# Performance work log

Hardware: AMD Instinct MI355X
Metric: run time of the kernel (lower is better)

The kernel has to match this reference:

```python
import jax, jax.numpy as jnp
import numpy as np

B, TP, TQ, DP, DQ, H, AH = 32, 512, 64, 256, 256, 256, 256
NL = 2  # len(nhids)
NEG = -1e9


def setup_inputs() -> dict:
    key = jax.random.key(0)
    ks = jax.random.split(key, 12)
    s = 0.05  # small init scale (stands in for xavier uniform)
    inp = {
        'input_p': jax.random.normal(ks[0], (B, TP, DP), jnp.float32),
        'mask_p': jnp.ones((B, TP), jnp.float32),
        'input_q': jax.random.normal(ks[1], (B, TQ, DQ), jnp.float32),
        'mask_q': jnp.ones((B, TQ), jnp.float32),
        # Match-LSTM attention params, stacked over depth (layer0 input dim DP == nhids[0] == 256)
        'W_att_p': jax.random.normal(ks[2], (NL, DP, AH), jnp.float32) * s,
        'W_att_q': jax.random.normal(ks[3], (NL, DQ, AH), jnp.float32) * s,
        'W_att_r': jax.random.normal(ks[4], (NL, H, AH), jnp.float32) * s,
        'w_att':   jax.random.normal(ks[5], (NL, AH), jnp.float32) * s,
        # LSTMCell: pre_act_linear over cat([input(=in_dim+DQ), h]) -> 4H; in_dim+DQ+H = 768 for both layers
        'W_lstm':  jax.random.normal(ks[6], (NL, DP + DQ + H, 4 * H), jnp.float32) * s,
        'bias_f':  jnp.ones((NL, H), jnp.float32),        # init.fill_(1.0)
        'bias_iog': jnp.zeros((NL, 3 * H), jnp.float32),  # init.fill_(0.0)
    }
    return inp


def reference(input_p, mask_p, input_q, mask_q,
              W_att_p, W_att_q, W_att_r, w_att,
              W_lstm, bias_f, bias_iog):
    bsz = input_p.shape[0]
    qmask_big = mask_q > 0  # (B,TQ) bool, reused every step
    x = input_p  # layer input, (B, TP, Din)
    for d in range(NL):
        qWq = jnp.einsum('btq,qa->bta', input_q, W_att_q[d])  # precompute (B,TQ,AH)
        Wp, Wr, wa = W_att_p[d], W_att_r[d], w_att[d]
        Wl = W_lstm[d]
        bias = jnp.concatenate([bias_f[d], bias_iog[d]])  # order: f | i,o,g

        def step(carry, xt_mt):
            h, c = carry
            xt, mt = xt_mt  # (B,Din), (B,)
            # match attention over query
            s = jnp.tanh(qWq + (xt @ Wp + h @ Wr)[:, None, :]) @ wa  # (B,TQ)
            alpha = jax.nn.softmax(jnp.where(qmask_big, s, NEG), axis=-1)
            z = jnp.einsum('bt,btd->bd', alpha, input_q)  # (B,DQ)
            # LSTM cell: pre_act over cat([attn_input, h])
            pre = jnp.concatenate([xt, z, h], axis=-1) @ Wl + bias
            f, i, o, g = jnp.split(pre, 4, axis=-1)
            m = mt[:, None]
            c1 = jax.nn.sigmoid(f) * c + jax.nn.sigmoid(i) * jnp.tanh(g)
            c1 = c1 * m + c * (1.0 - m)
            h1 = jax.nn.sigmoid(o) * jnp.tanh(c1)
            h1 = h1 * m + h * (1.0 - m)
            return (h1, c1), h1

        h0 = jnp.zeros((bsz, H), input_p.dtype)
        c0 = jnp.zeros((bsz, H), input_p.dtype)
        xs = (jnp.swapaxes(x, 0, 1), jnp.swapaxes(mask_p, 0, 1))  # time-major
        _, hs = jax.lax.scan(step, (h0, c0), xs)  # hs: (TP, B, H)
        x = jnp.swapaxes(hs, 0, 1)  # (B, TP, H), fed to next layer (dropout p=0)
    return x
```

## Files before the change

### kernel.cpp

```cpp
#include <hip/hip_runtime.h>
#include <hip/hip_bf16.h>


#define NB 32
#define TPL 512
#define TQL 64
#define DD 256
#define H4 1024
#define NC 1280
#define NS 8
#define SC 160
#define GC 128

typedef unsigned long long u64;

__device__ __forceinline__ float fast_tanh(float x) {
  float xc = fminf(fmaxf(x, -9.f), 9.f);
  float e = __expf(2.f * xc);
  return (e - 1.f) * __builtin_amdgcn_rcpf(e + 1.f);
}
__device__ __forceinline__ float fast_sigmoid(float x) {
  return __builtin_amdgcn_rcpf(1.f + __expf(-x));
}
__device__ __forceinline__ float bflo(unsigned int w) { return __uint_as_float(w << 16); }
__device__ __forceinline__ float bfhi(unsigned int w) { return __uint_as_float(w & 0xffff0000u); }
__device__ __forceinline__ unsigned int packbf(float a, float b) {
  unsigned int lo = __hip_bfloat16_raw(__float2bfloat16(a)).x;
  unsigned int hi = __hip_bfloat16_raw(__float2bfloat16(b)).x;
  return lo | (hi << 16);
}

__device__ __forceinline__ u64 aload64(const u64* p) {
  return __hip_atomic_load(p, __ATOMIC_RELAXED, __HIP_MEMORY_SCOPE_AGENT);
}
__device__ __forceinline__ void astore64(u64* p, u64 v) {
  __hip_atomic_store(p, v, __ATOMIC_RELAXED, __HIP_MEMORY_SCOPE_AGENT);
}
__device__ __forceinline__ u64 packsv(float val, unsigned int seq) {
  return ((u64)seq << 32) | (u64)__float_as_uint(val);
}
__device__ __forceinline__ float spinload(const u64* p, unsigned int seq) {
  u64 v = aload64(p);
  int guard = 0;
  while ((unsigned int)(v >> 32) != seq) {
    __builtin_amdgcn_s_sleep(1);
    v = aload64(p);
    if (++guard > (1 << 24)) break;
  }
  return __uint_as_float((unsigned int)v);
}

__device__ __forceinline__ int perm_col(int c) {
  if (c < DD) return (c >> 5) * SC + (c & 31);
  int cc = c - DD;
  int g = cc >> 8;
  int m = cc & 255;
  return (m >> 5) * SC + 32 + (g << 5) + (m & 31);
}

__global__ __launch_bounds__(256) void pack_weights(
    const float* __restrict__ Wp, const float* __restrict__ Wq,
    const float* __restrict__ Wl,
    float* __restrict__ wx, float* __restrict__ wqv)
{
  int d = blockIdx.y;
  int idx = blockIdx.x * 256 + threadIdx.x;
  if (idx >= DD * NC) return;
  int k = idx / NC, j = idx % NC;
  int o = d * DD * NC + idx;
  const float* Wld = Wl + (size_t)d * 768 * H4;
  if (j < DD) {
    int s = d * DD * DD + k * DD + j;
    wx[o] = Wp[s]; wqv[o] = Wq[s];
  } else {
    int c = j - DD;
    wx[o]  = Wld[(size_t)k * H4 + c];
    wqv[o] = Wld[(size_t)(DD + k) * H4 + c];
  }
}

__global__ __launch_bounds__(256) void pack_attl(
    const float* __restrict__ Wr, uint2* __restrict__ attl)
{
  int idx = blockIdx.x * 256 + threadIdx.x;
  if (idx >= 2 * NS * 4 * 512) return;
  int slot = idx & 511; int r = idx >> 9;
  int i = r & 3; r >>= 2;
  int j = r & 7; int d = r >> 3;
  int acol = slot & 31, ak = slot >> 5;
  int kq = ak * 4 + i;
  int col = (j << 5) + acol;
  float v[4];
  #pragma unroll
  for (int kr = 0; kr < 4; ++kr)
    v[kr] = Wr[((size_t)d * DD + kq * 4 + kr) * DD + col];
  attl[idx] = make_uint2(packbf(v[0], v[1]), packbf(v[2], v[3]));
}

__global__ __launch_bounds__(256) void pack_gatel(
    const float* __restrict__ Wl, uint2* __restrict__ gatel)
{
  int idx = blockIdx.x * 256 + threadIdx.x;
  if (idx >= 2 * NS * 16 * 512) return;
  int slot = idx & 511; int r = idx >> 9;
  int i = r & 15; r >>= 4;
  int j = r & 7; int d = r >> 3;
  int gcol = slot >> 2, gq = slot & 3;
  int kq = i * 4 + gq;
  int g = gcol >> 5, pos = gcol & 31;
  float v[4];
  #pragma unroll
  for (int kr = 0; kr < 4; ++kr) {
    int k = kq * 4 + kr;
    v[kr] = Wl[((size_t)d * 768 + 512 + k) * H4 + (g << 8) + (j << 5) + pos];
  }
  gatel[idx] = make_uint2(packbf(v[0], v[1]), packbf(v[2], v[3]));
}

template <bool PERM>
__global__ __launch_bounds__(256) void sgemm(
    const float* __restrict__ A, const float* __restrict__ Bm,
    float* __restrict__ C)
{
  __shared__ float As[16][65];
  __shared__ float Bs[16][64];
  int tid = threadIdx.x;
  int tx = tid & 15, ty = tid >> 4;
  int col0 = blockIdx.x * 64, row0 = blockIdx.y * 64;
  float acc[4][4] = {};
  for (int kt = 0; kt < DD; kt += 16) {
    #pragma unroll
    for (int i = 0; i < 4; ++i) {
      int e = tid + i * 256;
      As[e & 15][e >> 4] = A[(size_t)(row0 + (e >> 4)) * DD + kt + (e & 15)];
      Bs[e >> 6][e & 63] = Bm[(size_t)(kt + (e >> 6)) * NC + col0 + (e & 63)];
    }
    __syncthreads();
    #pragma unroll
    for (int kk = 0; kk < 16; ++kk) {
      float a[4], bv[4];
      #pragma unroll
      for (int i = 0; i < 4; ++i) a[i] = As[kk][ty * 4 + i];
      #pragma unroll
      for (int jj = 0; jj < 4; ++jj) bv[jj] = Bs[kk][tx * 4 + jj];
      #pragma unroll
      for (int i = 0; i < 4; ++i)
        #pragma unroll
        for (int jj = 0; jj < 4; ++jj)
          acc[i][jj] = fmaf(a[i], bv[jj], acc[i][jj]);
    }
    __syncthreads();
  }
  #pragma unroll
  for (int i = 0; i < 4; ++i)
    #pragma unroll
    for (int jj = 0; jj < 4; ++jj) {
      int c = col0 + tx * 4 + jj;
      int cc = PERM ? perm_col(c) : c;
      C[(size_t)(row0 + ty * 4 + i) * NC + cc] = acc[i][jj];
    }
}

__global__ __launch_bounds__(512, 1) void scan(
    const float* __restrict__ xpl,
    const float* __restrict__ qv,
    const uint2* __restrict__ attl,
    const uint2* __restrict__ gatel,
    const float* __restrict__ wa,
    const float* __restrict__ bias_f,
    const float* __restrict__ bias_iog,
    const float* __restrict__ mask_p,
    const float* __restrict__ mask_q,
    u64* __restrict__ xch_s,
    u64* __restrict__ xch_h,
    float* __restrict__ out,
    int lbase)
{
  const int bid = blockIdx.x;
  const int j = bid & 7, b = bid >> 3;
  const int tid = threadIdx.x;
  const int lane = tid & 63;

  __shared__ uint2 wg_l[16][512];
  __shared__ uint2 wat_l[4][512];
  __shared__ unsigned int vl_l[8][512];
  __shared__ float qT[32][65];
  __shared__ __align__(16) float h_lds[DD];
  __shared__ float xsl[SC];
  __shared__ float hw_att[32], waa[32], c_sh[32];
  __shared__ float att_part[16][33];
  __shared__ float sc_part[8][TQL];
  __shared__ float al_s[TQL];
  __shared__ float pre_s[GC], bias_s[GC];

  const float* qv_b = qv + (size_t)b * TQL * NC;
  u64* xch_s_b = xch_s + b * (NS * TQL);
  u64* xch_h_b = xch_h + b * DD;

  {
    const uint2* gp = gatel + (size_t)j * 16 * 512;
    for (int i = tid; i < 16 * 512; i += 512) wg_l[i >> 9][i & 511] = gp[i];
    const uint2* ap = attl + (size_t)j * 4 * 512;
    for (int i = tid; i < 4 * 512; i += 512) wat_l[i >> 9][i & 511] = ap[i];
    for (int i = tid; i < TQL * 32; i += 512) {
      int tq = i >> 5, a = i & 31;
      qT[a][tq] = qv_b[(size_t)tq * NC + (j << 5) + a];
    }
    for (int f = tid; f < 8 * 512; f += 512) {
      int ii = f >> 9, slot = f & 511;
      int gcol = slot >> 2, gq = slot & 3;
      int tw = gq * 8 + ii;
      int g = gcol >> 5, m = (j << 5) + (gcol & 31);
      float v0 = qv_b[(size_t)(2 * tw) * NC + DD + (g << 8) + m];
      float v1 = qv_b[(size_t)(2 * tw + 1) * NC + DD + (g << 8) + m];
      vl_l[ii][slot] = packbf(v0, v1);
    }
    if (tid < 32) { waa[tid] = wa[(j << 5) + tid]; c_sh[tid] = 0.f; }
    if (tid < GC) {
      int g = tid >> 5, m = (j << 5) + (tid & 31);
      bias_s[tid] = (g == 0) ? bias_f[m] : bias_iog[((g - 1) << 8) + m];
    }
  }
  float mq = mask_q[b * TQL + lane];
  __syncthreads();

  const int ak = tid >> 5;
  const int stq = tid & 63, ssub = tid >> 6;
  const int gcol = tid >> 2, gq = tid & 3;

  for (int t = 0; t < TPL; ++t) {
    const float* xrow = xpl + ((size_t)b * TPL + t) * NC + j * SC;
    float xv = (tid < SC) ? xrow[tid] : 0.f;
    const unsigned int hseq = (unsigned int)(lbase + t);
    const unsigned int sseq = (unsigned int)(lbase + t + 1);

    __syncthreads();
    if (tid < DD) h_lds[tid] = (t > 0) ? spinload(xch_h_b + tid, hseq) : 0.f;
    if (tid < SC) xsl[tid] = xv;
    __syncthreads();

    {
      float a0 = 0.f, a1 = 0.f;
      #pragma unroll
      for (int i = 0; i < 4; ++i) {
        int kq = ak * 4 + i;
        uint2 w = wat_l[i][tid];
        float4 h0 = *(const float4*)&h_lds[kq * 4];
        a0 = fmaf(h0.x, bflo(w.x), a0); a1 = fmaf(h0.y, bfhi(w.x), a1);
        a0 = fmaf(h0.z, bflo(w.y), a0); a1 = fmaf(h0.w, bfhi(w.y), a1);
      }
      att_part[ak][tid & 31] = a0 + a1;
    }
    __syncthreads();
    if (tid < 32) {
      float s = 0.f;
      #pragma unroll
      for (int i = 0; i < 16; ++i) s += att_part[i][tid];
      hw_att[tid] = s;
    }
    __syncthreads();

    {
      float p = 0.f;
      #pragma unroll
      for (int i = 0; i < 4; ++i) {
        int a = ssub * 4 + i;
        p = fmaf(fast_tanh(qT[a][stq] + xsl[a] + hw_att[a]), waa[a], p);
      }
      sc_part[ssub][stq] = p;
    }
    __syncthreads();
    if (tid < TQL) {
      float s = 0.f;
      #pragma unroll
      for (int q = 0; q < 8; ++q) s += sc_part[q][tid];
      astore64(xch_s_b + (j << 6) + tid, packsv(s, sseq));
    }

    float hwg;
    {
      float g0 = 0.f, g1 = 0.f;
      #pragma unroll
      for (int i = 0; i < 16; ++i) {
        int kq = i * 4 + gq;
        uint2 w = wg_l[i][tid];
        float4 h0 = *(const float4*)&h_lds[kq * 4];
        g0 = fmaf(h0.x, bflo(w.x), g0); g1 = fmaf(h0.y, bfhi(w.x), g1);
        g0 = fmaf(h0.z, bflo(w.y), g0); g1 = fmaf(h0.w, bfhi(w.y), g1);
      }
      hwg = g0 + g1;
      hwg += __shfl_xor(hwg, 1);
      hwg += __shfl_xor(hwg, 2);
    }

    __syncthreads();
    sc_part[ssub][stq] = spinload(xch_s_b + (ssub << 6) + stq, sseq);
    __syncthreads();
    if (tid < TQL) {
      float v = 0.f;
      #pragma unroll
      for (int q = 0; q < 8; ++q) v += sc_part[q][tid];
      v = (mq > 0.f) ? v : -1e9f;
      float m = v;
      #pragma unroll
      for (int off = 32; off > 0; off >>= 1) m = fmaxf(m, __shfl_xor(m, off));
      float p = __expf(v - m);
      float su = p;
      #pragma unroll
      for (int off = 32; off > 0; off >>= 1) su += __shfl_xor(su, off);
      al_s[tid] = p * __builtin_amdgcn_rcpf(su);
    }
    __syncthreads();

    {
      float d0 = 0.f, d1 = 0.f;
      #pragma unroll
      for (int i = 0; i < 8; ++i) {
        int tw = gq * 8 + i;
        unsigned int v = vl_l[i][tid];
        d0 = fmaf(al_s[2 * tw], bflo(v), d0);
        d1 = fmaf(al_s[2 * tw + 1], bfhi(v), d1);
      }
      float d = d0 + d1;
      d += __shfl_xor(d, 1);
      d += __shfl_xor(d, 2);
      if (gq == 0)
        pre_s[gcol] = hwg + d + xsl[32 + gcol] + bias_s[gcol];
    }
    __syncthreads();

    if (tid < 32) {
      float f  = pre_s[tid];
      float ii = pre_s[32 + tid];
      float oo = pre_s[64 + tid];
      float g  = pre_s[96 + tid];
      float mtv = mask_p[b * TPL + t];
      int m = (j << 5) + tid;
      float c0 = c_sh[tid], h0 = h_lds[m];
      float c1 = fast_sigmoid(f) * c0 + fast_sigmoid(ii) * fast_tanh(g);
      c1 = c1 * mtv + c0 * (1.f - mtv);
      float h1 = fast_sigmoid(oo) * fast_tanh(c1);
      h1 = h1 * mtv + h0 * (1.f - mtv);
      c_sh[tid] = c1;
      astore64(xch_h_b + m, packsv(h1, (unsigned int)(lbase + t + 1)));
      out[((size_t)b * TPL + t) * DD + m] = h1;
    }
  }
}

extern "C" void kernel_launch(void* const* d_in, const int* in_sizes, int n_in,
                              void* d_out, int out_size, void* d_ws, size_t ws_size,
                              hipStream_t stream) {
  const float* input_p  = (const float*)d_in[0];
  const float* mask_p   = (const float*)d_in[1];
  const float* input_q  = (const float*)d_in[2];
  const float* mask_q   = (const float*)d_in[3];
  const float* W_att_p  = (const float*)d_in[4];
  const float* W_att_q  = (const float*)d_in[5];
  const float* W_att_r  = (const float*)d_in[6];
  const float* w_att    = (const float*)d_in[7];
  const float* W_lstm   = (const float*)d_in[8];
  const float* bias_f   = (const float*)d_in[9];
  const float* bias_iog = (const float*)d_in[10];
  float* out = (float*)d_out;
  float* ws  = (float*)d_ws;
  (void)ws_size; (void)in_sizes; (void)n_in; (void)out_size;

  const size_t SZ_XPL  = (size_t)NB * TPL * NC;
  const size_t SZ_QV   = (size_t)NB * TQL * NC;
  const size_t SZ_W    = (size_t)DD * NC;
  const size_t SZ_ATTL = (size_t)NS * 4 * 512;
  const size_t SZ_GATL = (size_t)NS * 16 * 512;

  float* ws_xpl = ws;
  float* ws_qv  = ws_xpl + SZ_XPL;
  float* ws_wx  = ws_qv  + 2 * SZ_QV;
  float* ws_wqv = ws_wx  + 2 * SZ_W;
  float* ws_o0  = ws_wqv + 2 * SZ_W;
  uint2* ws_attl = (uint2*)(ws_o0 + (size_t)NB * TPL * DD);
  uint2* ws_gatl = ws_attl + 2 * SZ_ATTL;
  u64*   ws_xs   = (u64*)(ws_gatl + 2 * SZ_GATL);
  u64*   ws_xh   = ws_xs + NB * NS * TQL;

  dim3 gpack((DD * NC + 255) / 256, 2);
  pack_weights<<<gpack, 256, 0, stream>>>(W_att_p, W_att_q, W_lstm, ws_wx, ws_wqv);
  pack_attl<<<(2 * NS * 4 * 512 + 255) / 256, 256, 0, stream>>>(W_att_r, ws_attl);
  pack_gatel<<<(2 * NS * 16 * 512 + 255) / 256, 256, 0, stream>>>(W_lstm, ws_gatl);
  hipMemsetAsync(ws_xs, 0, (NB * NS * TQL + NB * DD) * sizeof(u64), stream);

  for (int d = 0; d < 2; ++d) {
    dim3 g(NC / 64, (NB * TQL) / 64);
    sgemm<false><<<g, 256, 0, stream>>>(input_q, ws_wqv + d * SZ_W, ws_qv + d * SZ_QV);
  }

  {
    dim3 g(NC / 64, (NB * TPL) / 64);
    sgemm<true><<<g, 256, 0, stream>>>(input_p, ws_wx, ws_xpl);
    scan<<<NB * NS, 512, 0, stream>>>(ws_xpl, ws_qv, ws_attl, ws_gatl,
                                      w_att, bias_f, bias_iog, mask_p, mask_q,
                                      ws_xs, ws_xh, ws_o0, 0);
  }
  {
    dim3 g(NC / 64, (NB * TPL) / 64);
    sgemm<true><<<g, 256, 0, stream>>>(ws_o0, ws_wx + SZ_W, ws_xpl);
    scan<<<NB * NS, 512, 0, stream>>>(ws_xpl, ws_qv + SZ_QV, ws_attl + SZ_ATTL,
                                      ws_gatl + SZ_GATL, w_att + DD, bias_f + DD,
                                      bias_iog + 3 * DD, mask_p, mask_q,
                                      ws_xs, ws_xh, out, TPL);
  }
}
```

Before: 4.021 ms.

## Process two batch rows per workgroup in the recurrent scan kernel

Each scan workgroup now handles two batch elements (b and b+16) for its column slice, halving the grid. LDS-resident weights are shared between the two rows, and the h/score exchange spinloads poll both rows together. Barriers are amortised over twice the work, and the cell state moves into a register. In exchange, the serial per-step compute in each workgroup roughly doubles, and LDS use grows.

```diff
diff --git a/kernel.cpp b/kernel.cpp
--- a/kernel.cpp
+++ b/kernel.cpp
@@ -39,15 +39,20 @@
 __device__ __forceinline__ u64 packsv(float val, unsigned int seq) {
   return ((u64)seq << 32) | (u64)__float_as_uint(val);
 }
-__device__ __forceinline__ float spinload(const u64* p, unsigned int seq) {
-  u64 v = aload64(p);
+__device__ __forceinline__ void spinload2(const u64* p0, const u64* p1,
+                                          unsigned int seq,
+                                          float* v0, float* v1) {
+  u64 a = aload64(p0);
+  u64 b = aload64(p1);
   int guard = 0;
-  while ((unsigned int)(v >> 32) != seq) {
+  while (((unsigned int)(a >> 32) != seq) || ((unsigned int)(b >> 32) != seq)) {
     __builtin_amdgcn_s_sleep(1);
-    v = aload64(p);
+    if ((unsigned int)(a >> 32) != seq) a = aload64(p0);
+    if ((unsigned int)(b >> 32) != seq) b = aload64(p1);
     if (++guard > (1 << 24)) break;
   }
-  return __uint_as_float((unsigned int)v);
+  *v0 = __uint_as_float((unsigned int)a);
+  *v1 = __uint_as_float((unsigned int)b);
 }
 
 __device__ __forceinline__ int perm_col(int c) {
@@ -176,52 +181,58 @@
     float* __restrict__ out,
     int lbase)
 {
-  const int bid = blockIdx.x;
-  const int j = bid & 7, b = bid >> 3;
+  const int wgid = blockIdx.x;
+  const int j = wgid & 7, pair = wgid >> 3;
   const int tid = threadIdx.x;
   const int lane = tid & 63;
+  const int bS0 = pair, bS1 = pair + 16;
 
   __shared__ uint2 wg_l[16][512];
   __shared__ uint2 wat_l[4][512];
-  __shared__ unsigned int vl_l[8][512];
-  __shared__ float qT[32][65];
-  __shared__ __align__(16) float h_lds[DD];
-  __shared__ float xsl[SC];
-  __shared__ float hw_att[32], waa[32], c_sh[32];
-  __shared__ float att_part[16][33];
-  __shared__ float sc_part[8][TQL];
-  __shared__ float al_s[TQL];
-  __shared__ float pre_s[GC], bias_s[GC];
-
-  const float* qv_b = qv + (size_t)b * TQL * NC;
-  u64* xch_s_b = xch_s + b * (NS * TQL);
-  u64* xch_h_b = xch_h + b * DD;
+  __shared__ unsigned int vl_l[2][8][512];
+  __shared__ float qT[2][32][65];
+  __shared__ __align__(16) float h_lds[2][DD];
+  __shared__ float xsl[2][SC];
+  __shared__ float hw_att[2][32], waa[32], c_dummy;
+  __shared__ float att_part[2][16][33];
+  __shared__ float sc_part[2][8][TQL];
+  __shared__ float al_s[2][TQL];
+  __shared__ float pre_s[2][GC], bias_s[GC];
+
+  const float* qvb[2] = { qv + (size_t)bS0 * TQL * NC,
+                          qv + (size_t)bS1 * TQL * NC };
+  u64* xsc[2] = { xch_s + bS0 * (NS * TQL), xch_s + bS1 * (NS * TQL) };
+  u64* xh[2]  = { xch_h + bS0 * DD,         xch_h + bS1 * DD };
 
   {
     const uint2* gp = gatel + (size_t)j * 16 * 512;
     for (int i = tid; i < 16 * 512; i += 512) wg_l[i >> 9][i & 511] = gp[i];
     const uint2* ap = attl + (size_t)j * 4 * 512;
     for (int i = tid; i < 4 * 512; i += 512) wat_l[i >> 9][i & 511] = ap[i];
-    for (int i = tid; i < TQL * 32; i += 512) {
-      int tq = i >> 5, a = i & 31;
-      qT[a][tq] = qv_b[(size_t)tq * NC + (j << 5) + a];
-    }
-    for (int f = tid; f < 8 * 512; f += 512) {
-      int ii = f >> 9, slot = f & 511;
-      int gcol = slot >> 2, gq = slot & 3;
-      int tw = gq * 8 + ii;
-      int g = gcol >> 5, m = (j << 5) + (gcol & 31);
-      float v0 = qv_b[(size_t)(2 * tw) * NC + DD + (g << 8) + m];
-      float v1 = qv_b[(size_t)(2 * tw + 1) * NC + DD + (g << 8) + m];
-      vl_l[ii][slot] = packbf(v0, v1);
-    }
-    if (tid < 32) { waa[tid] = wa[(j << 5) + tid]; c_sh[tid] = 0.f; }
+    #pragma unroll
+    for (int s = 0; s < 2; ++s) {
+      for (int i = tid; i < TQL * 32; i += 512) {
+        int tq = i >> 5, a = i & 31;
+        qT[s][a][tq] = qvb[s][(size_t)tq * NC + (j << 5) + a];
+      }
+      for (int f = tid; f < 8 * 512; f += 512) {
+        int ii = f >> 9, slot = f & 511;
+        int gcol = slot >> 2, gq = slot & 3;
+        int tw = gq * 8 + ii;
+        int g = gcol >> 5, m = (j << 5) + (gcol & 31);
+        float v0 = qvb[s][(size_t)(2 * tw) * NC + DD + (g << 8) + m];
+        float v1 = qvb[s][(size_t)(2 * tw + 1) * NC + DD + (g << 8) + m];
+        vl_l[s][ii][slot] = packbf(v0, v1);
+      }
+    }
+    if (tid < 32) waa[tid] = wa[(j << 5) + tid];
     if (tid < GC) {
       int g = tid >> 5, m = (j << 5) + (tid & 31);
       bias_s[tid] = (g == 0) ? bias_f[m] : bias_iog[((g - 1) << 8) + m];
     }
   }
-  float mq = mask_q[b * TQL + lane];
+  float mqv = (tid < 128) ? mask_q[((tid >> 6) ? bS1 : bS0) * TQL + lane] : 0.f;
+  float cv = 0.f;
   __syncthreads();
 
   const int ak = tid >> 5;
@@ -229,78 +240,102 @@
   const int gcol = tid >> 2, gq = tid & 3;
 
   for (int t = 0; t < TPL; ++t) {
-    const float* xrow = xpl + ((size_t)b * TPL + t) * NC + j * SC;
-    float xv = (tid < SC) ? xrow[tid] : 0.f;
+    const float* xrA = xpl + ((size_t)bS0 * TPL + t) * NC + j * SC;
+    const float* xrB = xpl + ((size_t)bS1 * TPL + t) * NC + j * SC;
+    float xv = 0.f;
+    if (tid < SC) xv = xrA[tid];
+    else if (tid < 2 * SC) xv = xrB[tid - SC];
+    float mtv = (tid < 64) ? mask_p[((lane >> 5) ? bS1 : bS0) * TPL + t] : 0.f;
     const unsigned int hseq = (unsigned int)(lbase + t);
     const unsigned int sseq = (unsigned int)(lbase + t + 1);
 
     __syncthreads();
-    if (tid < DD) h_lds[tid] = (t > 0) ? spinload(xch_h_b + tid, hseq) : 0.f;
-    if (tid < SC) xsl[tid] = xv;
-    __syncthreads();
-
-    {
+    if (tid < DD) {
+      float hA = 0.f, hB = 0.f;
+      if (t > 0) spinload2(xh[0] + tid, xh[1] + tid, hseq, &hA, &hB);
+      h_lds[0][tid] = hA;
+      h_lds[1][tid] = hB;
+    }
+    if (tid < SC) xsl[0][tid] = xv;
+    else if (tid < 2 * SC) xsl[1][tid - SC] = xv;
+    __syncthreads();
+
+    #pragma unroll
+    for (int s = 0; s < 2; ++s) {
       float a0 = 0.f, a1 = 0.f;
       #pragma unroll
       for (int i = 0; i < 4; ++i) {
         int kq = ak * 4 + i;
         uint2 w = wat_l[i][tid];
-        float4 h0 = *(const float4*)&h_lds[kq * 4];
+        float4 h0 = *(const float4*)&h_lds[s][kq * 4];
         a0 = fmaf(h0.x, bflo(w.x), a0); a1 = fmaf(h0.y, bfhi(w.x), a1);
         a0 = fmaf(h0.z, bflo(w.y), a0); a1 = fmaf(h0.w, bfhi(w.y), a1);
       }
-      att_part[ak][tid & 31] = a0 + a1;
-    }
-    __syncthreads();
-    if (tid < 32) {
-      float s = 0.f;
-      #pragma unroll
-      for (int i = 0; i < 16; ++i) s += att_part[i][tid];
-      hw_att[tid] = s;
-    }
-    __syncthreads();
-
-    {
+      att_part[s][ak][tid & 31] = a0 + a1;
+    }
+    __syncthreads();
+    if (tid < 64) {
+      int s = tid >> 5, e = tid & 31;
+      float sum = 0.f;
+      #pragma unroll
+      for (int i = 0; i < 16; ++i) sum += att_part[s][i][e];
+      hw_att[s][e] = sum;
+    }
+    __syncthreads();
+
+    #pragma unroll
+    for (int s = 0; s < 2; ++s) {
       float p = 0.f;
       #pragma unroll
       for (int i = 0; i < 4; ++i) {
         int a = ssub * 4 + i;
-        p = fmaf(fast_tanh(qT[a][stq] + xsl[a] + hw_att[a]), waa[a], p);
-      }
-      sc_part[ssub][stq] = p;
-    }
-    __syncthreads();
-    if (tid < TQL) {
-      float s = 0.f;
-      #pragma unroll
-      for (int q = 0; q < 8; ++q) s += sc_part[q][tid];
-      astore64(xch_s_b + (j << 6) + tid, packsv(s, sseq));
-    }
-
-    float hwg;
-    {
+        p = fmaf(fast_tanh(qT[s][a][stq] + xsl[s][a] + hw_att[s][a]),
+                 waa[a], p);
+      }
+      sc_part[s][ssub][stq] = p;
+    }
+    __syncthreads();
+    if (tid < 128) {
+      int s = tid >> 6;
+      float sum = 0.f;
+      #pragma unroll
+      for (int q = 0; q < 8; ++q) sum += sc_part[s][q][lane];
+      astore64(xsc[s] + (j << 6) + lane, packsv(sum, sseq));
+    }
+
+    float hwgA, hwgB;
+    #pragma unroll
+    for (int s = 0; s < 2; ++s) {
       float g0 = 0.f, g1 = 0.f;
       #pragma unroll
       for (int i = 0; i < 16; ++i) {
         int kq = i * 4 + gq;
         uint2 w = wg_l[i][tid];
-        float4 h0 = *(const float4*)&h_lds[kq * 4];
+        float4 h0 = *(const float4*)&h_lds[s][kq * 4];
         g0 = fmaf(h0.x, bflo(w.x), g0); g1 = fmaf(h0.y, bfhi(w.x), g1);
         g0 = fmaf(h0.z, bflo(w.y), g0); g1 = fmaf(h0.w, bfhi(w.y), g1);
       }
-      hwg = g0 + g1;
-      hwg += __shfl_xor(hwg, 1);
-      hwg += __shfl_xor(hwg, 2);
-    }
-
-    __syncthreads();
-    sc_part[ssub][stq] = spinload(xch_s_b + (ssub << 6) + stq, sseq);
-    __syncthreads();
-    if (tid < TQL) {
+      float hw = g0 + g1;
+      hw += __shfl_xor(hw, 1);
+      hw += __shfl_xor(hw, 2);
+      if (s == 0) hwgA = hw; else hwgB = hw;
+    }
+
+    __syncthreads();
+    {
+      float vA, vB;
+      spinload2(xsc[0] + (ssub << 6) + stq, xsc[1] + (ssub << 6) + stq,
+                sseq, &vA, &vB);
+      sc_part[0][ssub][stq] = vA;
+      sc_part[1][ssub][stq] = vB;
+    }
+    __syncthreads();
+    if (tid < 128) {
+      int s = tid >> 6;
       float v = 0.f;
       #pragma unroll
-      for (int q = 0; q < 8; ++q) v += sc_part[q][tid];
-      v = (mq > 0.f) ? v : -1e9f;
+      for (int q = 0; q < 8; ++q) v += sc_part[s][q][lane];
+      v = (mqv > 0.f) ? v : -1e9f;
       float m = v;
       #pragma unroll
       for (int off = 32; off > 0; off >>= 1) m = fmaxf(m, __shfl_xor(m, off));
@@ -308,44 +343,46 @@
       float su = p;
       #pragma unroll
       for (int off = 32; off > 0; off >>= 1) su += __shfl_xor(su, off);
-      al_s[tid] = p * __builtin_amdgcn_rcpf(su);
-    }
-    __syncthreads();
-
-    {
+      al_s[s][lane] = p * __builtin_amdgcn_rcpf(su);
+    }
+    __syncthreads();
+
+    #pragma unroll
+    for (int s = 0; s < 2; ++s) {
       float d0 = 0.f, d1 = 0.f;
       #pragma unroll
       for (int i = 0; i < 8; ++i) {
         int tw = gq * 8 + i;
-        unsigned int v = vl_l[i][tid];
-        d0 = fmaf(al_s[2 * tw], bflo(v), d0);
-        d1 = fmaf(al_s[2 * tw + 1], bfhi(v), d1);
+        unsigned int v = vl_l[s][i][tid];
+        d0 = fmaf(al_s[s][2 * tw], bflo(v), d0);
+        d1 = fmaf(al_s[s][2 * tw + 1], bfhi(v), d1);
       }
       float d = d0 + d1;
       d += __shfl_xor(d, 1);
       d += __shfl_xor(d, 2);
       if (gq == 0)
-        pre_s[gcol] = hwg + d + xsl[32 + gcol] + bias_s[gcol];
-    }
-    __syncthreads();
-
-    if (tid < 32) {
-      float f  = pre_s[tid];
-      float ii = pre_s[32 + tid];
-      float oo = pre_s[64 + tid];
-      float g  = pre_s[96 + tid];
-      float mtv = mask_p[b * TPL + t];
-      int m = (j << 5) + tid;
-      float c0 = c_sh[tid], h0 = h_lds[m];
+        pre_s[s][gcol] = (s ? hwgB : hwgA) + d + xsl[s][32 + gcol] + bias_s[gcol];
+    }
+    __syncthreads();
+
+    if (tid < 64) {
+      int s = lane >> 5, e = lane & 31;
+      float f  = pre_s[s][e];
+      float ii = pre_s[s][32 + e];
+      float oo = pre_s[s][64 + e];
+      float g  = pre_s[s][96 + e];
+      int m = (j << 5) + e;
+      float c0 = cv, h0 = h_lds[s][m];
       float c1 = fast_sigmoid(f) * c0 + fast_sigmoid(ii) * fast_tanh(g);
       c1 = c1 * mtv + c0 * (1.f - mtv);
       float h1 = fast_sigmoid(oo) * fast_tanh(c1);
       h1 = h1 * mtv + h0 * (1.f - mtv);
-      c_sh[tid] = c1;
-      astore64(xch_h_b + m, packsv(h1, (unsigned int)(lbase + t + 1)));
-      out[((size_t)b * TPL + t) * DD + m] = h1;
-    }
-  }
+      cv = c1;
+      astore64(xh[s] + m, packsv(h1, sseq));
+      out[((size_t)(s ? bS1 : bS0) * TPL + t) * DD + m] = h1;
+    }
+  }
+  (void)c_dummy;
 }
 
 extern "C" void kernel_launch(void* const* d_in, const int* in_sizes, int n_in,
@@ -396,16 +433,16 @@
   {
     dim3 g(NC / 64, (NB * TPL) / 64);
     sgemm<true><<<g, 256, 0, stream>>>(input_p, ws_wx, ws_xpl);
-    scan<<<NB * NS, 512, 0, stream>>>(ws_xpl, ws_qv, ws_attl, ws_gatl,
-                                      w_att, bias_f, bias_iog, mask_p, mask_q,
-                                      ws_xs, ws_xh, ws_o0, 0);
+    scan<<<NB * NS / 2, 512, 0, stream>>>(ws_xpl, ws_qv, ws_attl, ws_gatl,
+                                          w_att, bias_f, bias_iog, mask_p, mask_q,
+                                          ws_xs, ws_xh, ws_o0, 0);
   }
   {
     dim3 g(NC / 64, (NB * TPL) / 64);
     sgemm<true><<<g, 256, 0, stream>>>(ws_o0, ws_wx + SZ_W, ws_xpl);
-    scan<<<NB * NS, 512, 0, stream>>>(ws_xpl, ws_qv + SZ_QV, ws_attl + SZ_ATTL,
-                                      ws_gatl + SZ_GATL, w_att + DD, bias_f + DD,
-                                      bias_iog + 3 * DD, mask_p, mask_q,
-                                      ws_xs, ws_xh, out, TPL);
-  }
-}
+    scan<<<NB * NS / 2, 512, 0, stream>>>(ws_xpl, ws_qv + SZ_QV, ws_attl + SZ_ATTL,
+                                          ws_gatl + SZ_GATL, w_att + DD, bias_f + DD,
+                                          bias_iog + 3 * DD, mask_p, mask_q,
+                                          ws_xs, ws_xh, out, TPL);
+  }
+}
```

Result: slower. 5.079 ms (+26.3%).

## Cut per-step barriers in scan via shuffle reductions and redundant softmax

Applied to the files above, without the earlier changes.

The per-step recurrent loop is restructured to remove several __syncthreads. The h·Wr attention projection is now done by 256 threads with a shuffle reduction instead of an LDS partial-sum stage. Every wave now reads the local and remote score slices and computes the softmax redundantly, and alpha is broadcast by shuffles instead of through LDS. Cell state is kept in a register and the mask load is hoisted. The aim is to shorten the serial latency of each timestep. In exchange, each wave repeats the softmax work, and the Wr packing layout changes.

```diff
diff --git a/kernel.cpp b/kernel.cpp
--- a/kernel.cpp
+++ b/kernel.cpp
@@ -83,17 +83,16 @@
     const float* __restrict__ Wr, uint2* __restrict__ attl)
 {
   int idx = blockIdx.x * 256 + threadIdx.x;
-  if (idx >= 2 * NS * 4 * 512) return;
-  int slot = idx & 511; int r = idx >> 9;
-  int i = r & 3; r >>= 2;
+  if (idx >= 2 * NS * 8 * 256) return;
+  int tid = idx & 255; int r = idx >> 8;
+  int i = r & 7; r >>= 3;
   int j = r & 7; int d = r >> 3;
-  int acol = slot & 31, ak = slot >> 5;
-  int kq = ak * 4 + i;
-  int col = (j << 5) + acol;
+  int col = tid >> 3, q = tid & 7;
+  int kb = i * 32 + q * 4;
   float v[4];
   #pragma unroll
   for (int kr = 0; kr < 4; ++kr)
-    v[kr] = Wr[((size_t)d * DD + kq * 4 + kr) * DD + col];
+    v[kr] = Wr[((size_t)d * DD + kb + kr) * DD + (j << 5) + col];
   attl[idx] = make_uint2(packbf(v[0], v[1]), packbf(v[2], v[3]));
 }
 
@@ -182,15 +181,14 @@
   const int lane = tid & 63;
 
   __shared__ uint2 wg_l[16][512];
-  __shared__ uint2 wat_l[4][512];
+  __shared__ uint2 wat2[8][256];
   __shared__ unsigned int vl_l[8][512];
   __shared__ float qT[32][65];
   __shared__ __align__(16) float h_lds[DD];
   __shared__ float xsl[SC];
-  __shared__ float hw_att[32], waa[32], c_sh[32];
-  __shared__ float att_part[16][33];
+  __shared__ float hw_att[32], waa[32];
   __shared__ float sc_part[8][TQL];
-  __shared__ float al_s[TQL];
+  __shared__ float gat[7][TQL];
   __shared__ float pre_s[GC], bias_s[GC];
 
   const float* qv_b = qv + (size_t)b * TQL * NC;
@@ -200,8 +198,8 @@
   {
     const uint2* gp = gatel + (size_t)j * 16 * 512;
     for (int i = tid; i < 16 * 512; i += 512) wg_l[i >> 9][i & 511] = gp[i];
-    const uint2* ap = attl + (size_t)j * 4 * 512;
-    for (int i = tid; i < 4 * 512; i += 512) wat_l[i >> 9][i & 511] = ap[i];
+    const uint2* ap = attl + (size_t)j * 8 * 256;
+    for (int i = tid; i < 8 * 256; i += 512) wat2[i >> 8][i & 255] = ap[i];
     for (int i = tid; i < TQL * 32; i += 512) {
       int tq = i >> 5, a = i & 31;
       qT[a][tq] = qv_b[(size_t)tq * NC + (j << 5) + a];
@@ -215,22 +213,25 @@
       float v1 = qv_b[(size_t)(2 * tw + 1) * NC + DD + (g << 8) + m];
       vl_l[ii][slot] = packbf(v0, v1);
     }
-    if (tid < 32) { waa[tid] = wa[(j << 5) + tid]; c_sh[tid] = 0.f; }
+    if (tid < 32) waa[tid] = wa[(j << 5) + tid];
     if (tid < GC) {
       int g = tid >> 5, m = (j << 5) + (tid & 31);
       bias_s[tid] = (g == 0) ? bias_f[m] : bias_iog[((g - 1) << 8) + m];
     }
   }
   float mq = mask_q[b * TQL + lane];
+  float cv = 0.f;
   __syncthreads();
 
-  const int ak = tid >> 5;
   const int stq = tid & 63, ssub = tid >> 6;
   const int gcol = tid >> 2, gq = tid & 3;
+  const int sidx = (tid - 64) >> 6;
+  const int oslice = sidx + (sidx >= j ? 1 : 0);
 
   for (int t = 0; t < TPL; ++t) {
     const float* xrow = xpl + ((size_t)b * TPL + t) * NC + j * SC;
     float xv = (tid < SC) ? xrow[tid] : 0.f;
+    float mtv = (tid < 32) ? mask_p[b * TPL + t] : 0.f;
     const unsigned int hseq = (unsigned int)(lbase + t);
     const unsigned int sseq = (unsigned int)(lbase + t + 1);
 
@@ -239,24 +240,21 @@
     if (tid < SC) xsl[tid] = xv;
     __syncthreads();
 
-    {
+    if (tid < 256) {
+      int q = tid & 7;
       float a0 = 0.f, a1 = 0.f;
       #pragma unroll
-      for (int i = 0; i < 4; ++i) {
-        int kq = ak * 4 + i;
-        uint2 w = wat_l[i][tid];
-        float4 h0 = *(const float4*)&h_lds[kq * 4];
+      for (int i = 0; i < 8; ++i) {
+        uint2 w = wat2[i][tid];
+        float4 h0 = *(const float4*)&h_lds[i * 32 + q * 4];
         a0 = fmaf(h0.x, bflo(w.x), a0); a1 = fmaf(h0.y, bfhi(w.x), a1);
         a0 = fmaf(h0.z, bflo(w.y), a0); a1 = fmaf(h0.w, bfhi(w.y), a1);
       }
-      att_part[ak][tid & 31] = a0 + a1;
-    }
-    __syncthreads();
-    if (tid < 32) {
-      float s = 0.f;
-      #pragma unroll
-      for (int i = 0; i < 16; ++i) s += att_part[i][tid];
-      hw_att[tid] = s;
+      float p = a0 + a1;
+      p += __shfl_xor(p, 1);
+      p += __shfl_xor(p, 2);
+      p += __shfl_xor(p, 4);
+      if (q == 0) hw_att[tid >> 3] = p;
     }
     __syncthreads();
 
@@ -270,14 +268,14 @@
       sc_part[ssub][stq] = p;
     }
     __syncthreads();
-    if (tid < TQL) {
+
+    float hwg;
+    if (tid < 64) {
       float s = 0.f;
       #pragma unroll
       for (int q = 0; q < 8; ++q) s += sc_part[q][tid];
       astore64(xch_s_b + (j << 6) + tid, packsv(s, sseq));
     }
-
-    float hwg;
     {
       float g0 = 0.f, g1 = 0.f;
       #pragma unroll
@@ -292,14 +290,18 @@
       hwg += __shfl_xor(hwg, 1);
       hwg += __shfl_xor(hwg, 2);
     }
-
-    __syncthreads();
-    sc_part[ssub][stq] = spinload(xch_s_b + (ssub << 6) + stq, sseq);
-    __syncthreads();
-    if (tid < TQL) {
+    if (tid >= 64) {
+      gat[sidx][stq] = spinload(xch_s_b + (oslice << 6) + stq, sseq);
+    }
+    __syncthreads();
+
+    float al;
+    {
       float v = 0.f;
       #pragma unroll
-      for (int q = 0; q < 8; ++q) v += sc_part[q][tid];
+      for (int q = 0; q < 8; ++q) v += sc_part[q][lane];
+      #pragma unroll
+      for (int s = 0; s < 7; ++s) v += gat[s][lane];
       v = (mq > 0.f) ? v : -1e9f;
       float m = v;
       #pragma unroll
@@ -308,18 +310,18 @@
       float su = p;
       #pragma unroll
       for (int off = 32; off > 0; off >>= 1) su += __shfl_xor(su, off);
-      al_s[tid] = p * __builtin_amdgcn_rcpf(su);
-    }
-    __syncthreads();
-
+      al = p * __builtin_amdgcn_rcpf(su);
+    }
     {
       float d0 = 0.f, d1 = 0.f;
       #pragma unroll
       for (int i = 0; i < 8; ++i) {
         int tw = gq * 8 + i;
         unsigned int v = vl_l[i][tid];
-        d0 = fmaf(al_s[2 * tw], bflo(v), d0);
-        d1 = fmaf(al_s[2 * tw + 1], bfhi(v), d1);
+        float alo = __shfl(al, 2 * tw);
+        float ahi = __shfl(al, 2 * tw + 1);
+        d0 = fmaf(alo, bflo(v), d0);
+        d1 = fmaf(ahi, bfhi(v), d1);
       }
       float d = d0 + d1;
       d += __shfl_xor(d, 1);
@@ -334,15 +336,14 @@
       float ii = pre_s[32 + tid];
       float oo = pre_s[64 + tid];
       float g  = pre_s[96 + tid];
-      float mtv = mask_p[b * TPL + t];
       int m = (j << 5) + tid;
-      float c0 = c_sh[tid], h0 = h_lds[m];
+      float c0 = cv, h0 = h_lds[m];
       float c1 = fast_sigmoid(f) * c0 + fast_sigmoid(ii) * fast_tanh(g);
       c1 = c1 * mtv + c0 * (1.f - mtv);
       float h1 = fast_sigmoid(oo) * fast_tanh(c1);
       h1 = h1 * mtv + h0 * (1.f - mtv);
-      c_sh[tid] = c1;
-      astore64(xch_h_b + m, packsv(h1, (unsigned int)(lbase + t + 1)));
+      cv = c1;
+      astore64(xch_h_b + m, packsv(h1, sseq));
       out[((size_t)b * TPL + t) * DD + m] = h1;
     }
   }
@@ -369,7 +370,7 @@
   const size_t SZ_XPL  = (size_t)NB * TPL * NC;
   const size_t SZ_QV   = (size_t)NB * TQL * NC;
   const size_t SZ_W    = (size_t)DD * NC;
-  const size_t SZ_ATTL = (size_t)NS * 4 * 512;
+  const size_t SZ_ATTL = (size_t)NS * 8 * 256;
   const size_t SZ_GATL = (size_t)NS * 16 * 512;
 
   float* ws_xpl = ws;
@@ -384,7 +385,7 @@
 
   dim3 gpack((DD * NC + 255) / 256, 2);
   pack_weights<<<gpack, 256, 0, stream>>>(W_att_p, W_att_q, W_lstm, ws_wx, ws_wqv);
-  pack_attl<<<(2 * NS * 4 * 512 + 255) / 256, 256, 0, stream>>>(W_att_r, ws_attl);
+  pack_attl<<<(2 * NS * 8 * 256 + 255) / 256, 256, 0, stream>>>(W_att_r, ws_attl);
   pack_gatel<<<(2 * NS * 16 * 512 + 255) / 256, 256, 0, stream>>>(W_lstm, ws_gatl);
   hipMemsetAsync(ws_xs, 0, (NB * NS * TQL + NB * DD) * sizeof(u64), stream);
 
```

Result: slower. 4.308 ms (+7.1%).
